# Kernel tuning notes

Measured on AMD Instinct MI355X. Metric: run time of the kernel, lower is better.

## Reference

```python
import jax, jax.numpy as jnp
import numpy as np

B, T, D, F = 4, 1024, 256, 128  # input_dim=D, feature_dim=F, cat_size=1+F


def prelu(x, a):
    # torch.nn.PReLU with a single shared parameter (default init 0.25)
    return jnp.where(x >= 0, x, a * x)


def setup_inputs() -> dict:
    key = jax.random.key(0)
    ks = jax.random.split(key, 10)
    cat = 1 + F
    s1 = 1.0 / np.sqrt(cat)
    s2 = 1.0 / np.sqrt(F)
    return {
        "input": jax.random.normal(ks[0], (B, T, D), jnp.float32),
        "feature": jax.random.normal(ks[1], (B, T, F), jnp.float32),
        "slider": jax.random.uniform(ks[2], (B, T, 1), jnp.float32),
        "W1": jax.random.uniform(ks[3], (F, cat), jnp.float32, -s1, s1),
        "b1": jax.random.uniform(ks[4], (F,), jnp.float32, -s1, s1),
        "a1": jnp.float32(0.25),
        "W2": jax.random.uniform(ks[5], (F, F), jnp.float32, -s2, s2),
        "b2": jax.random.uniform(ks[6], (F,), jnp.float32, -s2, s2),
        "a2": jnp.float32(0.25),
        "Wp": jax.random.uniform(ks[7], (2, cat), jnp.float32, -s1, s1),
        "bp": jax.random.uniform(ks[8], (2,), jnp.float32, -s1, s1),
    }


def reference(input, feature, slider, W1, b1, a1, W2, b2, a2, Wp, bp):
    # input: (B,T,D) -> (B,T,D,1); feature broadcast over D: (B,T,1,F)
    inp = input[..., None]                       # (B,T,D,1)
    feat = feature[..., None, :]                 # (B,T,1,F)
    feat = jnp.broadcast_to(feat, (B, T, D, F))  # repeat across input_dim
    x = jnp.concatenate((inp, feat), axis=-1)    # (B,T,D,1+F)
    # tmlp: Linear -> PReLU -> Linear -> PReLU
    h = prelu(jnp.einsum('btdc,fc->btdf', x, W1) + b1, a1)  # (B,T,D,F)
    h = prelu(jnp.einsum('btdf,gf->btdg', h, W2) + b2, a2)  # (B,T,D,F)
    y = jnp.concatenate((h, inp), axis=-1)       # (B,T,D,1+F)
    p = jnp.einsum('btdc,oc->btdo', y, Wp) + bp  # (B,T,D,2)
    g = p[..., 0:1] * jax.nn.sigmoid(p[..., 1:2])  # GLU(dim=-1) -> (B,T,D,1)
    return (inp * (1.0 + g)).squeeze(-1)         # (B,T,D)
```

## Files before the change

kernel.cpp:

```cpp
#include <hip/hip_runtime.h>
#include <hip/hip_bf16.h>

#define BT 4096
#define DD 256
#define CAT 129

typedef __attribute__((ext_vector_type(8))) _Float16 f16x8;
typedef __attribute__((ext_vector_type(4))) _Float16 f16x4;
typedef __attribute__((ext_vector_type(2))) _Float16 h2;
typedef __attribute__((ext_vector_type(4))) float f32x4;

#define PIN(x) asm volatile("" : "+v"(x))

static __device__ __forceinline__ h2 cvt_pk(float a, float b) {
    return __builtin_bit_cast(h2, __builtin_amdgcn_cvt_pkrtz(a, b));
}

static __device__ __forceinline__ float fdot2f(h2 a, h2 b, float c) {
#if __has_builtin(__builtin_amdgcn_fdot2)
    return __builtin_amdgcn_fdot2(__builtin_bit_cast(__fp16 __attribute__((ext_vector_type(2))), a),
                                  __builtin_bit_cast(__fp16 __attribute__((ext_vector_type(2))), b),
                                  c, false);
#else
    return fmaf((float)a[0], (float)b[0], fmaf((float)a[1], (float)b[1], c));
#endif
}

__global__ void __launch_bounds__(256) k_cvt(
    const float* __restrict__ W1, const float* __restrict__ W2,
    _Float16* __restrict__ w2h, _Float16* __restrict__ w1h,
    _Float16* __restrict__ w10h)
{
    const int t = threadIdx.x, b = blockIdx.x;
    if (b < 8) {
        #pragma unroll
        for (int i = 0; i < 8; ++i) {
            int idx = b * 2048 + i * 256 + t;
            w2h[idx] = (_Float16)W2[idx];
        }
    } else {
        int q = b - 8;
        #pragma unroll
        for (int i = 0; i < 8; ++i) {
            int idx = q * 2048 + i * 256 + t;
            int f = idx >> 7, c = idx & 127;
            w1h[idx ^ ((f & 7) << 3)] = (_Float16)W1[f * CAT + 1 + c];
        }
        if (q == 0 && t < 128) w10h[t] = (_Float16)W1[t * CAT];
    }
}

__global__ void __launch_bounds__(256) k_prep2(
    const float* __restrict__ feature, const _Float16* __restrict__ w1h,
    const float* __restrict__ b1p, _Float16* __restrict__ v1h)
{
    __shared__ __align__(16) _Float16 fS[2048];
    const int t = threadIdx.x;
    const int r0 = blockIdx.x * 16;

    {
        int e = t * 8;
        int r = e >> 7, c = e & 127;
        const float4* src = (const float4*)(feature + (size_t)(r0 + r) * 128 + c);
        float4 x0 = src[0], x1 = src[1];
        f16x8 hv;
        hv[0] = (_Float16)x0.x; hv[1] = (_Float16)x0.y;
        hv[2] = (_Float16)x0.z; hv[3] = (_Float16)x0.w;
        hv[4] = (_Float16)x1.x; hv[5] = (_Float16)x1.y;
        hv[6] = (_Float16)x1.z; hv[7] = (_Float16)x1.w;
        *(f16x8*)&fS[e ^ ((r & 7) << 3)] = hv;
    }
    __syncthreads();

    const int lane = t & 63, wv = t >> 6;
    const int l15 = lane & 15, l4 = lane >> 4;

    f16x8 bfr[2][4];
    float4 b1v[2];
    #pragma unroll
    for (int nt = 0; nt < 2; ++nt) {
        const int f0 = wv * 32 + nt * 16;
        b1v[nt] = *(const float4*)(b1p + f0 + l4 * 4);
        #pragma unroll
        for (int kc = 0; kc < 4; ++kc) {
            int f = f0 + l15, c = kc * 32 + l4 * 8;
            bfr[nt][kc] = *(const f16x8*)&w1h[(f * 128 + c) ^ ((f & 7) << 3)];
        }
    }

    const f32x4 fz = {0.f, 0.f, 0.f, 0.f};
    f32x4 acc[2] = {fz, fz};
    #pragma unroll
    for (int kc = 0; kc < 4; ++kc) {
        int r = l15, c = kc * 32 + l4 * 8;
        f16x8 afr = *(const f16x8*)&fS[(r * 128 + c) ^ ((r & 7) << 3)];
        #pragma unroll
        for (int nt = 0; nt < 2; ++nt)
            acc[nt] = __builtin_amdgcn_mfma_f32_16x16x32_f16(
                bfr[nt][kc], afr, acc[nt], 0, 0, 0);
    }

    #pragma unroll
    for (int nt = 0; nt < 2; ++nt) {
        f16x4 o;
        o[0] = (_Float16)(acc[nt][0] + ((const float*)&b1v[nt])[0]);
        o[1] = (_Float16)(acc[nt][1] + ((const float*)&b1v[nt])[1]);
        o[2] = (_Float16)(acc[nt][2] + ((const float*)&b1v[nt])[2]);
        o[3] = (_Float16)(acc[nt][3] + ((const float*)&b1v[nt])[3]);
        *(f16x4*)&v1h[(size_t)(r0 + l15) * 128 + wv * 32 + nt * 16 + l4 * 4] = o;
    }
}

__global__ void __launch_bounds__(256, 3) k_main(
    const float* __restrict__ inp, const float* __restrict__ b2p,
    const float* __restrict__ Wp, const float* __restrict__ a1p,
    const float* __restrict__ a2p, const _Float16* __restrict__ v1h,
    const _Float16* __restrict__ w2h, const _Float16* __restrict__ w10h,
    unsigned* __restrict__ pr)
{
    const int tid  = threadIdx.x;
    const int lane = tid & 63, wv = tid >> 6;
    const int l15  = lane & 15, l4 = lane >> 4;
    const int W    = blockIdx.x * 4 + wv;
    const int cg   = W & 1, bt = W >> 1;

    f16x8 bfr[4][4];
    #pragma unroll
    for (int nt = 0; nt < 4; ++nt)
        #pragma unroll
        for (int kc = 0; kc < 4; ++kc) {
            bfr[nt][kc] = *(const f16x8*)
                &w2h[(cg * 64 + nt * 16 + l15) * 128 + kc * 32 + l4 * 8];
            PIN(bfr[nt][kc]);
        }

    f16x8 v1pk[4], w10pk[4];
    #pragma unroll
    for (int kc = 0; kc < 4; ++kc) {
        v1pk[kc]  = *(const f16x8*)&v1h[(size_t)bt * 128 + kc * 32 + l4 * 8];
        w10pk[kc] = *(const f16x8*)&w10h[kc * 32 + l4 * 8];
        PIN(v1pk[kc]); PIN(w10pk[kc]);
    }

    f32x4 accInit[4];
    h2 wpapk[4][2], wpbpk[4][2];
    #pragma unroll
    for (int nt = 0; nt < 4; ++nt) {
        const int g0 = cg * 64 + nt * 16 + l4 * 4;
        const float4 bv = *(const float4*)&b2p[g0];
        const float4 wa = *(const float4*)&Wp[g0];
        accInit[nt][0] = bv.x; accInit[nt][1] = bv.y;
        accInit[nt][2] = bv.z; accInit[nt][3] = bv.w;
        wpapk[nt][0] = cvt_pk(wa.x, wa.y);  wpapk[nt][1] = cvt_pk(wa.z, wa.w);
        wpbpk[nt][0] = cvt_pk(Wp[CAT + g0],     Wp[CAT + g0 + 1]);
        wpbpk[nt][1] = cvt_pk(Wp[CAT + g0 + 2], Wp[CAT + g0 + 3]);
        PIN(accInit[nt]);
        PIN(wpapk[nt][0]); PIN(wpapk[nt][1]);
        PIN(wpbpk[nt][0]); PIN(wpbpk[nt][1]);
    }

    const _Float16 a1s = (_Float16)a1p[0];
    const _Float16 a2s = (_Float16)a2p[0];
    f16x8 a1x8 = {a1s, a1s, a1s, a1s, a1s, a1s, a1s, a1s};
    h2 a2v; a2v[0] = a2s; a2v[1] = a2s;
    PIN(a1x8); PIN(a2v);

    const float* srow = inp + (size_t)bt * DD;
    float s_cur = srow[l15];

    #pragma unroll 2
    for (int it = 0; it < 16; ++it) {
        const float s_row = s_cur;
        if (it < 15) s_cur = srow[(it + 1) * 16 + l15];

        const _Float16 sh = (_Float16)s_row;
        const f16x8 s8 = {sh, sh, sh, sh, sh, sh, sh, sh};

        f32x4 acc[4];
        #pragma unroll
        for (int kc = 0; kc < 4; ++kc) {
            f16x8 h  = v1pk[kc] + w10pk[kc] * s8;
            f16x8 af = __builtin_elementwise_max(h, a1x8 * h);
            #pragma unroll
            for (int nt = 0; nt < 4; ++nt)
                acc[nt] = __builtin_amdgcn_mfma_f32_16x16x32_f16(
                    bfr[nt][kc], af, (kc == 0) ? accInit[nt] : acc[nt], 0, 0, 0);
        }

        float p0 = 0.f, p1 = 0.f;
        #pragma unroll
        for (int nt = 0; nt < 4; ++nt) {
            h2 hh0 = cvt_pk(acc[nt][0], acc[nt][1]);
            h2 hh1 = cvt_pk(acc[nt][2], acc[nt][3]);
            h2 hp0 = __builtin_elementwise_max(hh0, a2v * hh0);
            h2 hp1 = __builtin_elementwise_max(hh1, a2v * hh1);
            p0 = fdot2f(wpapk[nt][0], hp0, p0);
            p0 = fdot2f(wpapk[nt][1], hp1, p0);
            p1 = fdot2f(wpbpk[nt][0], hp0, p1);
            p1 = fdot2f(wpbpk[nt][1], hp1, p1);
        }

        p0 += __shfl_xor(p0, 16); p0 += __shfl_xor(p0, 32);
        p1 += __shfl_xor(p1, 16); p1 += __shfl_xor(p1, 32);

        if (l4 == 0)
            pr[((size_t)bt * DD + it * 16 + l15) * 2 + cg] =
                __builtin_bit_cast(unsigned, cvt_pk(p0, p1));
    }
}

__global__ void __launch_bounds__(256) k_fin(
    const float* __restrict__ inp, const float* __restrict__ Wp,
    const float* __restrict__ bpp, const unsigned* __restrict__ pr,
    float* __restrict__ out)
{
    const int i = blockIdx.x * 256 + threadIdx.x;
    const float wpi0 = Wp[128], wpi1 = Wp[CAT + 128];
    const float bp0  = bpp[0],  bp1  = bpp[1];

    const uint2 v = ((const uint2*)pr)[i];
    const h2 pa = __builtin_bit_cast(h2, v.x);
    const h2 pb = __builtin_bit_cast(h2, v.y);
    const float s = inp[i];

    const float e0 = (float)pa[0] + (float)pb[0] + wpi0 * s + bp0;
    const float e1 = (float)pa[1] + (float)pb[1] + wpi1 * s + bp1;
    const float gg = e0 / (1.f + __expf(-e1));
    out[i] = s * (1.f + gg);
}

extern "C" void kernel_launch(void* const* d_in, const int* in_sizes, int n_in,
                              void* d_out, int out_size, void* d_ws, size_t ws_size,
                              hipStream_t stream)
{
    (void)in_sizes; (void)n_in; (void)out_size; (void)ws_size;
    const float* input   = (const float*)d_in[0];
    const float* feature = (const float*)d_in[1];
    const float* W1 = (const float*)d_in[3];
    const float* b1 = (const float*)d_in[4];
    const float* a1 = (const float*)d_in[5];
    const float* W2 = (const float*)d_in[6];
    const float* b2 = (const float*)d_in[7];
    const float* a2 = (const float*)d_in[8];
    const float* Wp = (const float*)d_in[9];
    const float* bp = (const float*)d_in[10];
    float* out = (float*)d_out;

    unsigned*  pr   = (unsigned*)d_ws;
    _Float16*  v1h  = (_Float16*)((char*)d_ws + (size_t)BT * DD * 8);
    _Float16*  w2h  = v1h + (size_t)BT * 128;
    _Float16*  w1h  = w2h + 16384;
    _Float16*  w10h = w1h + 16384;

    k_cvt  <<<dim3(16),   dim3(256), 0, stream>>>(W1, W2, w2h, w1h, w10h);
    k_prep2<<<dim3(256),  dim3(256), 0, stream>>>(feature, w1h, b1, v1h);
    k_main <<<dim3(2048), dim3(256), 0, stream>>>(input, b2, Wp, a1, a2,
                                                  v1h, w2h, w10h, pr);
    k_fin  <<<dim3(4096), dim3(256), 0, stream>>>(input, Wp, bp, pr, out);
}
```

Baseline: 66.84 us.

## Process two row tiles per iteration and defer cross-lane reduction to finalize kernel

The main kernel now handles two 16-row tiles per loop iteration, interleaving their MFMA chains to give more independent work per wave. It drops the shuffle-based reduction across the four lane groups: every lane group writes its own packed partial to one of 8 planes, and the finalize kernel sums the 8 partials. This removes the shuffles and the predicated store but multiplies partial-sum traffic to the workspace by four and doubles register pressure, so the launch bound drops to 2 waves-per-EU occupancy.

```diff
diff --git a/kernel.cpp b/kernel.cpp
--- a/kernel.cpp
+++ b/kernel.cpp
@@ -111,7 +111,7 @@
     }
 }
 
-__global__ void __launch_bounds__(256, 3) k_main(
+__global__ void __launch_bounds__(256, 2) k_main(
     const float* __restrict__ inp, const float* __restrict__ b2p,
     const float* __restrict__ Wp, const float* __restrict__ a1p,
     const float* __restrict__ a2p, const _Float16* __restrict__ v1h,
@@ -161,51 +161,73 @@
 
     const _Float16 a1s = (_Float16)a1p[0];
     const _Float16 a2s = (_Float16)a2p[0];
-    f16x8 a1x8 = {a1s, a1s, a1s, a1s, a1s, a1s, a1s, a1s};
+    const f16x8 a1x8 = {a1s, a1s, a1s, a1s, a1s, a1s, a1s, a1s};
     h2 a2v; a2v[0] = a2s; a2v[1] = a2s;
-    PIN(a1x8); PIN(a2v);
 
     const float* srow = inp + (size_t)bt * DD;
-    float s_cur = srow[l15];
+    unsigned* prw = pr + (size_t)(cg * 4 + l4) * (BT * DD) + (size_t)bt * DD;
 
     #pragma unroll 2
-    for (int it = 0; it < 16; ++it) {
-        const float s_row = s_cur;
-        if (it < 15) s_cur = srow[(it + 1) * 16 + l15];
-
-        const _Float16 sh = (_Float16)s_row;
-        const f16x8 s8 = {sh, sh, sh, sh, sh, sh, sh, sh};
-
-        f32x4 acc[4];
+    for (int it = 0; it < 8; ++it) {
+        const float sAf = srow[it * 32 + l15];
+        const float sBf = srow[it * 32 + 16 + l15];
+        const _Float16 shA = (_Float16)sAf, shB = (_Float16)sBf;
+        const f16x8 s8A = {shA, shA, shA, shA, shA, shA, shA, shA};
+        const f16x8 s8B = {shB, shB, shB, shB, shB, shB, shB, shB};
+
+        f32x4 accA[4], accB[4];
         #pragma unroll
         for (int kc = 0; kc < 4; ++kc) {
-            f16x8 h  = v1pk[kc] + w10pk[kc] * s8;
-            f16x8 af = __builtin_elementwise_max(h, a1x8 * h);
+            f16x8 hA  = v1pk[kc] + w10pk[kc] * s8A;
+            f16x8 afA = __builtin_elementwise_max(hA, a1x8 * hA);
+            f16x8 hB  = v1pk[kc] + w10pk[kc] * s8B;
+            f16x8 afB = __builtin_elementwise_max(hB, a1x8 * hB);
             #pragma unroll
-            for (int nt = 0; nt < 4; ++nt)
-                acc[nt] = __builtin_amdgcn_mfma_f32_16x16x32_f16(
-                    bfr[nt][kc], af, (kc == 0) ? accInit[nt] : acc[nt], 0, 0, 0);
-        }
-
-        float p0 = 0.f, p1 = 0.f;
+            for (int nt = 0; nt < 4; ++nt) {
+                accA[nt] = __builtin_amdgcn_mfma_f32_16x16x32_f16(
+                    bfr[nt][kc], afA, (kc == 0) ? accInit[nt] : accA[nt], 0, 0, 0);
+                accB[nt] = __builtin_amdgcn_mfma_f32_16x16x32_f16(
+                    bfr[nt][kc], afB, (kc == 0) ? accInit[nt] : accB[nt], 0, 0, 0);
+            }
+        }
+
+        float p0Aa = 0.f, p0Ab = 0.f, p1Aa = 0.f, p1Ab = 0.f;
+        float p0Ba = 0.f, p0Bb = 0.f, p1Ba = 0.f, p1Bb = 0.f;
         #pragma unroll
         for (int nt = 0; nt < 4; ++nt) {
-            h2 hh0 = cvt_pk(acc[nt][0], acc[nt][1]);
-            h2 hh1 = cvt_pk(acc[nt][2], acc[nt][3]);
-            h2 hp0 = __builtin_elementwise_max(hh0, a2v * hh0);
-            h2 hp1 = __builtin_elementwise_max(hh1, a2v * hh1);
-            p0 = fdot2f(wpapk[nt][0], hp0, p0);
-            p0 = fdot2f(wpapk[nt][1], hp1, p0);
-            p1 = fdot2f(wpbpk[nt][0], hp0, p1);
-            p1 = fdot2f(wpbpk[nt][1], hp1, p1);
-        }
-
-        p0 += __shfl_xor(p0, 16); p0 += __shfl_xor(p0, 32);
-        p1 += __shfl_xor(p1, 16); p1 += __shfl_xor(p1, 32);
-
-        if (l4 == 0)
-            pr[((size_t)bt * DD + it * 16 + l15) * 2 + cg] =
-                __builtin_bit_cast(unsigned, cvt_pk(p0, p1));
+            h2 hA0 = cvt_pk(accA[nt][0], accA[nt][1]);
+            h2 hA1 = cvt_pk(accA[nt][2], accA[nt][3]);
+            h2 pA0 = __builtin_elementwise_max(hA0, a2v * hA0);
+            h2 pA1 = __builtin_elementwise_max(hA1, a2v * hA1);
+            h2 hB0 = cvt_pk(accB[nt][0], accB[nt][1]);
+            h2 hB1 = cvt_pk(accB[nt][2], accB[nt][3]);
+            h2 pB0 = __builtin_elementwise_max(hB0, a2v * hB0);
+            h2 pB1 = __builtin_elementwise_max(hB1, a2v * hB1);
+            if (nt < 2) {
+                p0Aa = fdot2f(wpapk[nt][0], pA0, p0Aa);
+                p0Aa = fdot2f(wpapk[nt][1], pA1, p0Aa);
+                p1Aa = fdot2f(wpbpk[nt][0], pA0, p1Aa);
+                p1Aa = fdot2f(wpbpk[nt][1], pA1, p1Aa);
+                p0Ba = fdot2f(wpapk[nt][0], pB0, p0Ba);
+                p0Ba = fdot2f(wpapk[nt][1], pB1, p0Ba);
+                p1Ba = fdot2f(wpbpk[nt][0], pB0, p1Ba);
+                p1Ba = fdot2f(wpbpk[nt][1], pB1, p1Ba);
+            } else {
+                p0Ab = fdot2f(wpapk[nt][0], pA0, p0Ab);
+                p0Ab = fdot2f(wpapk[nt][1], pA1, p0Ab);
+                p1Ab = fdot2f(wpbpk[nt][0], pA0, p1Ab);
+                p1Ab = fdot2f(wpbpk[nt][1], pA1, p1Ab);
+                p0Bb = fdot2f(wpapk[nt][0], pB0, p0Bb);
+                p0Bb = fdot2f(wpapk[nt][1], pB1, p0Bb);
+                p1Bb = fdot2f(wpbpk[nt][0], pB0, p1Bb);
+                p1Bb = fdot2f(wpbpk[nt][1], pB1, p1Bb);
+            }
+        }
+
+        prw[it * 32 + l15] =
+            __builtin_bit_cast(unsigned, cvt_pk(p0Aa + p0Ab, p1Aa + p1Ab));
+        prw[it * 32 + 16 + l15] =
+            __builtin_bit_cast(unsigned, cvt_pk(p0Ba + p0Bb, p1Ba + p1Bb));
     }
 }
 
@@ -218,13 +240,16 @@
     const float wpi0 = Wp[128], wpi1 = Wp[CAT + 128];
     const float bp0  = bpp[0],  bp1  = bpp[1];
 
-    const uint2 v = ((const uint2*)pr)[i];
-    const h2 pa = __builtin_bit_cast(h2, v.x);
-    const h2 pb = __builtin_bit_cast(h2, v.y);
+    float e0 = 0.f, e1 = 0.f;
+    #pragma unroll
+    for (int p = 0; p < 8; ++p) {
+        const h2 v = __builtin_bit_cast(h2, pr[(size_t)p * (BT * DD) + i]);
+        e0 += (float)v[0];
+        e1 += (float)v[1];
+    }
     const float s = inp[i];
-
-    const float e0 = (float)pa[0] + (float)pb[0] + wpi0 * s + bp0;
-    const float e1 = (float)pa[1] + (float)pb[1] + wpi1 * s + bp1;
+    e0 += wpi0 * s + bp0;
+    e1 += wpi1 * s + bp1;
     const float gg = e0 / (1.f + __expf(-e1));
     out[i] = s * (1.f + gg);
 }
@@ -247,7 +272,7 @@
     float* out = (float*)d_out;
 
     unsigned*  pr   = (unsigned*)d_ws;
-    _Float16*  v1h  = (_Float16*)((char*)d_ws + (size_t)BT * DD * 8);
+    _Float16*  v1h  = (_Float16*)((char*)d_ws + (size_t)8 * BT * DD * 4);
     _Float16*  w2h  = v1h + (size_t)BT * 128;
     _Float16*  w1h  = w2h + 16384;
     _Float16*  w10h = w1h + 16384;
```

Result: slower. 72.04 us (+7.8%).

## Interleave two row groups per iteration in k_main with packed-f16 inline asm

Applied to the files above, without the earlier changes.

The main loop now handles two 16-row groups per iteration, issuing two independent MFMA accumulator chains so their latencies overlap. The PReLU and bias math uses explicit v_pk_fma/v_pk_mul/v_pk_max asm on packed u32 values. All 16 slider values are preloaded and packed up front, and the Wp dot-product accumulators are split to shorten dependency chains. Launch bounds drop occupancy from 3 to 2 blocks to make room for the extra registers, which may cost latency hiding.

```diff
diff --git a/kernel.cpp b/kernel.cpp
--- a/kernel.cpp
+++ b/kernel.cpp
@@ -6,23 +6,40 @@
 #define CAT 129
 
 typedef __attribute__((ext_vector_type(8))) _Float16 f16x8;
-typedef __attribute__((ext_vector_type(4))) _Float16 f16x4;
 typedef __attribute__((ext_vector_type(2))) _Float16 h2;
+typedef __attribute__((ext_vector_type(2))) __fp16 fp16x2;
 typedef __attribute__((ext_vector_type(4))) float f32x4;
+typedef __attribute__((ext_vector_type(4))) unsigned u32x4;
+typedef unsigned u32;
 
 #define PIN(x) asm volatile("" : "+v"(x))
 
+static __device__ __forceinline__ u32 pk_fma(u32 a, u32 b, u32 c) {
+    u32 d; asm("v_pk_fma_f16 %0, %1, %2, %3" : "=v"(d) : "v"(a), "v"(b), "v"(c));
+    return d;
+}
+static __device__ __forceinline__ u32 pk_mul(u32 a, u32 b) {
+    u32 d; asm("v_pk_mul_f16 %0, %1, %2" : "=v"(d) : "v"(a), "v"(b));
+    return d;
+}
+static __device__ __forceinline__ u32 pk_max(u32 a, u32 b) {
+    u32 d; asm("v_pk_max_f16 %0, %1, %2" : "=v"(d) : "v"(a), "v"(b));
+    return d;
+}
+
+static __device__ __forceinline__ u32 cvtpk_u(float a, float b) {
+    return __builtin_bit_cast(u32, __builtin_amdgcn_cvt_pkrtz(a, b));
+}
 static __device__ __forceinline__ h2 cvt_pk(float a, float b) {
     return __builtin_bit_cast(h2, __builtin_amdgcn_cvt_pkrtz(a, b));
 }
-
-static __device__ __forceinline__ float fdot2f(h2 a, h2 b, float c) {
+static __device__ __forceinline__ float fdot2u(u32 a, u32 b, float c) {
 #if __has_builtin(__builtin_amdgcn_fdot2)
-    return __builtin_amdgcn_fdot2(__builtin_bit_cast(__fp16 __attribute__((ext_vector_type(2))), a),
-                                  __builtin_bit_cast(__fp16 __attribute__((ext_vector_type(2))), b),
-                                  c, false);
+    return __builtin_amdgcn_fdot2(__builtin_bit_cast(fp16x2, a),
+                                  __builtin_bit_cast(fp16x2, b), c, false);
 #else
-    return fmaf((float)a[0], (float)b[0], fmaf((float)a[1], (float)b[1], c));
+    h2 x = __builtin_bit_cast(h2, a), y = __builtin_bit_cast(h2, b);
+    return fmaf((float)x[0], (float)y[0], fmaf((float)x[1], (float)y[1], c));
 #endif
 }
 
@@ -102,21 +119,22 @@
 
     #pragma unroll
     for (int nt = 0; nt < 2; ++nt) {
-        f16x4 o;
-        o[0] = (_Float16)(acc[nt][0] + ((const float*)&b1v[nt])[0]);
-        o[1] = (_Float16)(acc[nt][1] + ((const float*)&b1v[nt])[1]);
-        o[2] = (_Float16)(acc[nt][2] + ((const float*)&b1v[nt])[2]);
-        o[3] = (_Float16)(acc[nt][3] + ((const float*)&b1v[nt])[3]);
-        *(f16x4*)&v1h[(size_t)(r0 + l15) * 128 + wv * 32 + nt * 16 + l4 * 4] = o;
-    }
-}
-
-__global__ void __launch_bounds__(256, 3) k_main(
+        h2 o01 = cvt_pk(acc[nt][0] + ((const float*)&b1v[nt])[0],
+                        acc[nt][1] + ((const float*)&b1v[nt])[1]);
+        h2 o23 = cvt_pk(acc[nt][2] + ((const float*)&b1v[nt])[2],
+                        acc[nt][3] + ((const float*)&b1v[nt])[3]);
+        _Float16* dst = v1h + (size_t)(r0 + l15) * 128 + wv * 32 + nt * 16 + l4 * 4;
+        *(h2*)dst = o01;
+        *(h2*)(dst + 2) = o23;
+    }
+}
+
+__global__ void __launch_bounds__(256, 2) k_main(
     const float* __restrict__ inp, const float* __restrict__ b2p,
     const float* __restrict__ Wp, const float* __restrict__ a1p,
     const float* __restrict__ a2p, const _Float16* __restrict__ v1h,
     const _Float16* __restrict__ w2h, const _Float16* __restrict__ w10h,
-    unsigned* __restrict__ pr)
+    u32* __restrict__ pr)
 {
     const int tid  = threadIdx.x;
     const int lane = tid & 63, wv = tid >> 6;
@@ -134,16 +152,16 @@
             PIN(bfr[nt][kc]);
         }
 
-    f16x8 v1pk[4], w10pk[4];
+    u32x4 v1q[4], w10q[4];
     #pragma unroll
     for (int kc = 0; kc < 4; ++kc) {
-        v1pk[kc]  = *(const f16x8*)&v1h[(size_t)bt * 128 + kc * 32 + l4 * 8];
-        w10pk[kc] = *(const f16x8*)&w10h[kc * 32 + l4 * 8];
-        PIN(v1pk[kc]); PIN(w10pk[kc]);
+        v1q[kc]  = *(const u32x4*)&v1h[(size_t)bt * 128 + kc * 32 + l4 * 8];
+        w10q[kc] = *(const u32x4*)&w10h[kc * 32 + l4 * 8];
+        PIN(v1q[kc]); PIN(w10q[kc]);
     }
 
     f32x4 accInit[4];
-    h2 wpapk[4][2], wpbpk[4][2];
+    u32 wpapk[4][2], wpbpk[4][2];
     #pragma unroll
     for (int nt = 0; nt < 4; ++nt) {
         const int g0 = cg * 64 + nt * 16 + l4 * 4;
@@ -151,67 +169,107 @@
         const float4 wa = *(const float4*)&Wp[g0];
         accInit[nt][0] = bv.x; accInit[nt][1] = bv.y;
         accInit[nt][2] = bv.z; accInit[nt][3] = bv.w;
-        wpapk[nt][0] = cvt_pk(wa.x, wa.y);  wpapk[nt][1] = cvt_pk(wa.z, wa.w);
-        wpbpk[nt][0] = cvt_pk(Wp[CAT + g0],     Wp[CAT + g0 + 1]);
-        wpbpk[nt][1] = cvt_pk(Wp[CAT + g0 + 2], Wp[CAT + g0 + 3]);
+        wpapk[nt][0] = cvtpk_u(wa.x, wa.y);  wpapk[nt][1] = cvtpk_u(wa.z, wa.w);
+        wpbpk[nt][0] = cvtpk_u(Wp[CAT + g0],     Wp[CAT + g0 + 1]);
+        wpbpk[nt][1] = cvtpk_u(Wp[CAT + g0 + 2], Wp[CAT + g0 + 3]);
         PIN(accInit[nt]);
         PIN(wpapk[nt][0]); PIN(wpapk[nt][1]);
         PIN(wpbpk[nt][0]); PIN(wpbpk[nt][1]);
     }
 
-    const _Float16 a1s = (_Float16)a1p[0];
-    const _Float16 a2s = (_Float16)a2p[0];
-    f16x8 a1x8 = {a1s, a1s, a1s, a1s, a1s, a1s, a1s, a1s};
-    h2 a2v; a2v[0] = a2s; a2v[1] = a2s;
-    PIN(a1x8); PIN(a2v);
+    const float a1f = a1p[0], a2f = a2p[0];
+    u32 a1pk = cvtpk_u(a1f, a1f);
+    u32 a2pk = cvtpk_u(a2f, a2f);
+    PIN(a1pk); PIN(a2pk);
 
     const float* srow = inp + (size_t)bt * DD;
-    float s_cur = srow[l15];
-
-    #pragma unroll 2
-    for (int it = 0; it < 16; ++it) {
-        const float s_row = s_cur;
-        if (it < 15) s_cur = srow[(it + 1) * 16 + l15];
-
-        const _Float16 sh = (_Float16)s_row;
-        const f16x8 s8 = {sh, sh, sh, sh, sh, sh, sh, sh};
-
-        f32x4 acc[4];
+    u32 s2[16];
+    #pragma unroll
+    for (int i = 0; i < 16; ++i) {
+        const float sv = srow[i * 16 + l15];
+        s2[i] = cvtpk_u(sv, sv);
+        PIN(s2[i]);
+    }
+
+    u32* prw = pr + ((size_t)bt * DD) * 2 + cg;
+
+    #pragma unroll
+    for (int it = 0; it < 8; ++it) {
+        const u32 sA = s2[2 * it], sB = s2[2 * it + 1];
+
+        f32x4 accA[4], accB[4];
         #pragma unroll
         for (int kc = 0; kc < 4; ++kc) {
-            f16x8 h  = v1pk[kc] + w10pk[kc] * s8;
-            f16x8 af = __builtin_elementwise_max(h, a1x8 * h);
+            u32x4 afA, afB;
             #pragma unroll
-            for (int nt = 0; nt < 4; ++nt)
-                acc[nt] = __builtin_amdgcn_mfma_f32_16x16x32_f16(
-                    bfr[nt][kc], af, (kc == 0) ? accInit[nt] : acc[nt], 0, 0, 0);
-        }
-
-        float p0 = 0.f, p1 = 0.f;
+            for (int j = 0; j < 4; ++j) {
+                u32 hA = pk_fma(w10q[kc][j], sA, v1q[kc][j]);
+                afA[j] = pk_max(hA, pk_mul(a1pk, hA));
+                u32 hB = pk_fma(w10q[kc][j], sB, v1q[kc][j]);
+                afB[j] = pk_max(hB, pk_mul(a1pk, hB));
+            }
+            const f16x8 a8A = __builtin_bit_cast(f16x8, afA);
+            const f16x8 a8B = __builtin_bit_cast(f16x8, afB);
+            #pragma unroll
+            for (int nt = 0; nt < 4; ++nt) {
+                accA[nt] = __builtin_amdgcn_mfma_f32_16x16x32_f16(
+                    bfr[nt][kc], a8A, (kc == 0) ? accInit[nt] : accA[nt], 0, 0, 0);
+                accB[nt] = __builtin_amdgcn_mfma_f32_16x16x32_f16(
+                    bfr[nt][kc], a8B, (kc == 0) ? accInit[nt] : accB[nt], 0, 0, 0);
+            }
+        }
+
+        float p0Aa = 0.f, p0Ab = 0.f, p1Aa = 0.f, p1Ab = 0.f;
+        float p0Ba = 0.f, p0Bb = 0.f, p1Ba = 0.f, p1Bb = 0.f;
         #pragma unroll
         for (int nt = 0; nt < 4; ++nt) {
-            h2 hh0 = cvt_pk(acc[nt][0], acc[nt][1]);
-            h2 hh1 = cvt_pk(acc[nt][2], acc[nt][3]);
-            h2 hp0 = __builtin_elementwise_max(hh0, a2v * hh0);
-            h2 hp1 = __builtin_elementwise_max(hh1, a2v * hh1);
-            p0 = fdot2f(wpapk[nt][0], hp0, p0);
-            p0 = fdot2f(wpapk[nt][1], hp1, p0);
-            p1 = fdot2f(wpbpk[nt][0], hp0, p1);
-            p1 = fdot2f(wpbpk[nt][1], hp1, p1);
-        }
-
-        p0 += __shfl_xor(p0, 16); p0 += __shfl_xor(p0, 32);
-        p1 += __shfl_xor(p1, 16); p1 += __shfl_xor(p1, 32);
-
-        if (l4 == 0)
-            pr[((size_t)bt * DD + it * 16 + l15) * 2 + cg] =
-                __builtin_bit_cast(unsigned, cvt_pk(p0, p1));
+            u32 hA0 = cvtpk_u(accA[nt][0], accA[nt][1]);
+            u32 hA1 = cvtpk_u(accA[nt][2], accA[nt][3]);
+            u32 pA0 = pk_max(hA0, pk_mul(a2pk, hA0));
+            u32 pA1 = pk_max(hA1, pk_mul(a2pk, hA1));
+            u32 hB0 = cvtpk_u(accB[nt][0], accB[nt][1]);
+            u32 hB1 = cvtpk_u(accB[nt][2], accB[nt][3]);
+            u32 pB0 = pk_max(hB0, pk_mul(a2pk, hB0));
+            u32 pB1 = pk_max(hB1, pk_mul(a2pk, hB1));
+            if (nt < 2) {
+                p0Aa = fdot2u(wpapk[nt][0], pA0, p0Aa);
+                p0Aa = fdot2u(wpapk[nt][1], pA1, p0Aa);
+                p1Aa = fdot2u(wpbpk[nt][0], pA0, p1Aa);
+                p1Aa = fdot2u(wpbpk[nt][1], pA1, p1Aa);
+                p0Ba = fdot2u(wpapk[nt][0], pB0, p0Ba);
+                p0Ba = fdot2u(wpapk[nt][1], pB1, p0Ba);
+                p1Ba = fdot2u(wpbpk[nt][0], pB0, p1Ba);
+                p1Ba = fdot2u(wpbpk[nt][1], pB1, p1Ba);
+            } else {
+                p0Ab = fdot2u(wpapk[nt][0], pA0, p0Ab);
+                p0Ab = fdot2u(wpapk[nt][1], pA1, p0Ab);
+                p1Ab = fdot2u(wpbpk[nt][0], pA0, p1Ab);
+                p1Ab = fdot2u(wpbpk[nt][1], pA1, p1Ab);
+                p0Bb = fdot2u(wpapk[nt][0], pB0, p0Bb);
+                p0Bb = fdot2u(wpapk[nt][1], pB1, p0Bb);
+                p1Bb = fdot2u(wpbpk[nt][0], pB0, p1Bb);
+                p1Bb = fdot2u(wpbpk[nt][1], pB1, p1Bb);
+            }
+        }
+
+        float p0A = p0Aa + p0Ab, p1A = p1Aa + p1Ab;
+        float p0B = p0Ba + p0Bb, p1B = p1Ba + p1Bb;
+
+        p0A += __shfl_xor(p0A, 16); p0A += __shfl_xor(p0A, 32);
+        p1A += __shfl_xor(p1A, 16); p1A += __shfl_xor(p1A, 32);
+        p0B += __shfl_xor(p0B, 16); p0B += __shfl_xor(p0B, 32);
+        p1B += __shfl_xor(p1B, 16); p1B += __shfl_xor(p1B, 32);
+
+        if (l4 == 0) {
+            prw[(it * 32 + l15) * 2]        = cvtpk_u(p0A, p1A);
+            prw[(it * 32 + 16 + l15) * 2]   = cvtpk_u(p0B, p1B);
+        }
     }
 }
 
 __global__ void __launch_bounds__(256) k_fin(
     const float* __restrict__ inp, const float* __restrict__ Wp,
-    const float* __restrict__ bpp, const unsigned* __restrict__ pr,
+    const float* __restrict__ bpp, const u32* __restrict__ pr,
     float* __restrict__ out)
 {
     const int i = blockIdx.x * 256 + threadIdx.x;
@@ -246,7 +304,7 @@
     const float* bp = (const float*)d_in[10];
     float* out = (float*)d_out;
 
-    unsigned*  pr   = (unsigned*)d_ws;
+    u32*       pr   = (u32*)d_ws;
     _Float16*  v1h  = (_Float16*)((char*)d_ws + (size_t)BT * DD * 8);
     _Float16*  w2h  = v1h + (size_t)BT * 128;
     _Float16*  w1h  = w2h + 16384;
```

Measured after the change: 69.08 us. 1.03x slower.
